# Performance work log

Hardware: AMD Instinct MI355X
Metric: run time of the kernel (lower is better)

Reference implementation:

```python
import jax, jax.numpy as jnp
import numpy as np

N_NODES = 100000
N_EDGES = 1600000
D_IN = 128
D_HID = 128


def _sage_conv(x, src, dst, n_nodes, W_l, b_l, W_r):
    # mean-aggregate source-node features onto destination nodes
    msg = x[src]  # [E, d] gather
    agg = jax.ops.segment_sum(msg, dst, num_segments=n_nodes)  # [N, d]
    deg = jax.ops.segment_sum(jnp.ones((src.shape[0],), x.dtype), dst,
                              num_segments=n_nodes)  # [N]
    agg = agg / jnp.maximum(deg, 1.0)[:, None]
    # lin_l(agg) + lin_r(x)  (lin_r has no bias, as in PyG SAGEConv)
    return agg @ W_l + b_l + x @ W_r


def setup_inputs() -> dict:
    key = jax.random.key(0)
    ks = jax.random.split(key, 8)
    x = jax.random.normal(ks[0], (N_NODES, D_IN), dtype=jnp.float32)
    edge_index = jax.random.randint(ks[1], (2, N_EDGES), 0, N_NODES, dtype=jnp.int32)
    s_in = 1.0 / np.sqrt(D_IN)
    s_hid = 1.0 / np.sqrt(D_HID)
    return {
        "x": x,
        "edge_index": edge_index,
        "W1_l": jax.random.normal(ks[2], (D_IN, D_HID), jnp.float32) * s_in,
        "b1_l": jnp.zeros((D_HID,), jnp.float32),
        "W1_r": jax.random.normal(ks[3], (D_IN, D_HID), jnp.float32) * s_in,
        "W2_l": jax.random.normal(ks[4], (D_HID, D_HID), jnp.float32) * s_hid,
        "b2_l": jnp.zeros((D_HID,), jnp.float32),
        "W2_r": jax.random.normal(ks[5], (D_HID, D_HID), jnp.float32) * s_hid,
    }


def reference(x, edge_index, W1_l, b1_l, W1_r, W2_l, b2_l, W2_r):
    src, dst = edge_index[0], edge_index[1]
    h = _sage_conv(x, src, dst, x.shape[0], W1_l, b1_l, W1_r)
    h = jax.nn.relu(h)
    # dropout inactive in eval mode
    h = _sage_conv(h, src, dst, x.shape[0], W2_l, b2_l, W2_r)
    return h
```

## Files before the change

### kernel.cpp

```cpp
#include <hip/hip_runtime.h>
#include <hip/hip_bf16.h>
#include <stdint.h>

typedef short short8 __attribute__((ext_vector_type(8)));
typedef float floatx4 __attribute__((ext_vector_type(4)));
typedef int intx4 __attribute__((ext_vector_type(4)));

#define NSEG 8
#define BLK_PER_SEG 256
#define SLOT 32
#define SPILL 32

static __device__ __forceinline__ unsigned short f2bf(float f) {
    union { float f; unsigned u; } v; v.f = f;
    unsigned r = v.u + 0x7FFF + ((v.u >> 16) & 1);
    return (unsigned short)(r >> 16);
}
static __device__ __forceinline__ float bflo(unsigned u) {
    union { unsigned u; float f; } v; v.u = u << 16; return v.f;
}
static __device__ __forceinline__ float bfhi(unsigned u) {
    union { unsigned u; float f; } v; v.u = u & 0xFFFF0000u; return v.f;
}

__global__ void k_conv_x(const float4* __restrict__ x, ushort4* __restrict__ o, int n4) {
    int t = blockIdx.x * blockDim.x + threadIdx.x;
    if (t >= n4) return;
    float4 v = x[t];
    ushort4 r = { f2bf(v.x), f2bf(v.y), f2bf(v.z), f2bf(v.w) };
    o[t] = r;
}

__global__ void k_trans_w(const float* __restrict__ W1l, const float* __restrict__ W1r,
                          const float* __restrict__ W2l, const float* __restrict__ W2r,
                          ushort* __restrict__ wt1, ushort* __restrict__ wt2) {
    int t = blockIdx.x * blockDim.x + threadIdx.x;
    int m = t >> 15, r = t & 32767;
    int k = r >> 7, n = r & 127;
    const float* Wl = m ? W2l : W1l;
    const float* Wr = m ? W2r : W1r;
    float v = (k < 128) ? Wl[k * 128 + n] : Wr[(k - 128) * 128 + n];
    ushort* wt = m ? wt2 : wt1;
    wt[n * 256 + k] = f2bf(v);
}

static __device__ __forceinline__ int seg_of(int d, float inv_nps) {
    int s = (int)((float)d * inv_nps);
    return s > (NSEG - 1) ? (NSEG - 1) : s;
}

static __device__ __forceinline__ void put_slot(int d, int s, int* __restrict__ cnt,
                                                int* __restrict__ slots,
                                                int* __restrict__ spill) {
    int p = atomicAdd(&cnt[d], 1);
    if (p < SLOT) slots[(size_t)d * SLOT + p] = s;
    else          spill[(size_t)d * SPILL + (p - SLOT)] = s;
}

__global__ void __launch_bounds__(256)
k_build(const int* __restrict__ src, const int* __restrict__ dst,
        int* __restrict__ cnt, int* __restrict__ slots, int* __restrict__ spill,
        int E, float inv_nps) {
    int seg  = blockIdx.x & 7;
    int bseg = blockIdx.x >> 3;
    int e4tot = E >> 2;
    int ec4 = (e4tot + BLK_PER_SEG - 1) / BLK_PER_SEG;
    int start4 = bseg * ec4, end4 = min(e4tot, start4 + ec4);
    const intx4* d4 = (const intx4*)dst;
    const intx4* s4 = (const intx4*)src;
    for (int i = start4 + (int)threadIdx.x; i < end4; i += 256) {
        intx4 dv = __builtin_nontemporal_load(&d4[i]);
        intx4 sv = __builtin_nontemporal_load(&s4[i]);
        if (seg_of(dv.x, inv_nps) == seg) put_slot(dv.x, sv.x, cnt, slots, spill);
        if (seg_of(dv.y, inv_nps) == seg) put_slot(dv.y, sv.y, cnt, slots, spill);
        if (seg_of(dv.z, inv_nps) == seg) put_slot(dv.z, sv.z, cnt, slots, spill);
        if (seg_of(dv.w, inv_nps) == seg) put_slot(dv.w, sv.w, cnt, slots, spill);
    }
    if (bseg == BLK_PER_SEG - 1 && (int)threadIdx.x < (E & 3)) {
        int e = (e4tot << 2) + threadIdx.x;
        int d = dst[e];
        if (seg_of(d, inv_nps) == seg) put_slot(d, src[e], cnt, slots, spill);
    }
}

__global__ void __launch_bounds__(256)
k_agg(const ushort* __restrict__ h, const int* __restrict__ cnt,
      const int* __restrict__ slots, const int* __restrict__ spill,
      ushort* __restrict__ agg, int n) {
    int node = (blockIdx.x * 256 + threadIdx.x) >> 6;
    int lane = threadIdx.x & 63;
    if (node >= n) return;
    int eg = lane >> 4;
    int c8 = lane & 15;
    int deg = cnt[node];
    const int* sl = slots + (size_t)node * SLOT;
    const int* sp = spill + (size_t)node * SPILL;
    float a[8];
    #pragma unroll
    for (int i = 0; i < 8; ++i) a[i] = 0.f;
    const ushort* hb = h + (size_t)c8 * 8;
    for (int j = 0; j < deg; j += 16) {
        int b0 = j + eg * 4;
        const int* ip = (b0 < SLOT) ? (sl + b0) : (sp + (b0 - SLOT));
        uint4 iv = *(const uint4*)ip;
        uint4 u0 = {0,0,0,0}, u1 = {0,0,0,0}, u2 = {0,0,0,0}, u3 = {0,0,0,0};
        if (b0     < deg) u0 = *(const uint4*)(hb + (size_t)iv.x * 128);
        if (b0 + 1 < deg) u1 = *(const uint4*)(hb + (size_t)iv.y * 128);
        if (b0 + 2 < deg) u2 = *(const uint4*)(hb + (size_t)iv.z * 128);
        if (b0 + 3 < deg) u3 = *(const uint4*)(hb + (size_t)iv.w * 128);
        a[0] += bflo(u0.x) + bflo(u1.x) + bflo(u2.x) + bflo(u3.x);
        a[1] += bfhi(u0.x) + bfhi(u1.x) + bfhi(u2.x) + bfhi(u3.x);
        a[2] += bflo(u0.y) + bflo(u1.y) + bflo(u2.y) + bflo(u3.y);
        a[3] += bfhi(u0.y) + bfhi(u1.y) + bfhi(u2.y) + bfhi(u3.y);
        a[4] += bflo(u0.z) + bflo(u1.z) + bflo(u2.z) + bflo(u3.z);
        a[5] += bfhi(u0.z) + bfhi(u1.z) + bfhi(u2.z) + bfhi(u3.z);
        a[6] += bflo(u0.w) + bflo(u1.w) + bflo(u2.w) + bflo(u3.w);
        a[7] += bfhi(u0.w) + bfhi(u1.w) + bfhi(u2.w) + bfhi(u3.w);
    }
    #pragma unroll
    for (int m = 16; m < 64; m <<= 1) {
        #pragma unroll
        for (int i = 0; i < 8; ++i) a[i] += __shfl_xor(a[i], m);
    }
    if (eg == 0) {
        float inv = 1.0f / fmaxf((float)deg, 1.0f);
        uint4 o;
        o.x = (unsigned)f2bf(a[0] * inv) | ((unsigned)f2bf(a[1] * inv) << 16);
        o.y = (unsigned)f2bf(a[2] * inv) | ((unsigned)f2bf(a[3] * inv) << 16);
        o.z = (unsigned)f2bf(a[4] * inv) | ((unsigned)f2bf(a[5] * inv) << 16);
        o.w = (unsigned)f2bf(a[6] * inv) | ((unsigned)f2bf(a[7] * inv) << 16);
        *(uint4*)(agg + (size_t)node * 128 + c8 * 8) = o;
    }
}

__global__ void __launch_bounds__(256)
k_gemm(const ushort* __restrict__ A1, const ushort* __restrict__ A2,
       const ushort* __restrict__ wt, const float* __restrict__ bias,
       int M, int mode, ushort* __restrict__ out16, float* __restrict__ out32) {
    __shared__ ushort W[128 * 264];
    int tid = threadIdx.x;
    #pragma unroll
    for (int i = 0; i < 16; ++i) {
        int t = tid + i * 256;
        int nrow = t >> 5, k8 = t & 31;
        *(uint4*)&W[nrow * 264 + k8 * 8] = *(const uint4*)&wt[nrow * 256 + k8 * 8];
    }
    __syncthreads();
    int wave = tid >> 6, lane = tid & 63;
    int l15 = lane & 15, lg = lane >> 4;
    int row_base = blockIdx.x * 64 + wave * 16;
    int r = row_base + l15;
    int rc = min(r, M - 1);
    const ushort* a1 = A1 + (size_t)rc * 128;
    const ushort* a2 = A2 + (size_t)rc * 128;
    int kg = lg * 8;
    floatx4 acc[8];
    #pragma unroll
    for (int c = 0; c < 8; ++c) acc[c] = (floatx4){0.f, 0.f, 0.f, 0.f};
    #pragma unroll
    for (int ks = 0; ks < 8; ++ks) {
        int k0 = ks * 32 + kg;
        const ushort* ap = (ks < 4) ? (a1 + k0) : (a2 + (k0 - 128));
        short8 a = *(const short8*)ap;
        #pragma unroll
        for (int c = 0; c < 8; ++c) {
            short8 b = *(const short8*)&W[(c * 16 + l15) * 264 + k0];
            acc[c] = __builtin_amdgcn_mfma_f32_16x16x32_bf16(a, b, acc[c], 0, 0, 0);
        }
    }
    #pragma unroll
    for (int c = 0; c < 8; ++c) {
        int coln = c * 16 + l15;
        float bv = bias[coln];
        #pragma unroll
        for (int i = 0; i < 4; ++i) {
            int row = row_base + lg * 4 + i;
            if (row < M) {
                float v = acc[c][i] + bv;
                if (mode == 0) {
                    v = fmaxf(v, 0.f);
                    out16[(size_t)row * 128 + coln] = f2bf(v);
                } else {
                    out32[(size_t)row * 128 + coln] = v;
                }
            }
        }
    }
}

extern "C" void kernel_launch(void* const* d_in, const int* in_sizes, int n_in,
                              void* d_out, int out_size, void* d_ws, size_t ws_size,
                              hipStream_t stream) {
    const float* x   = (const float*)d_in[0];
    const int*   ei  = (const int*)d_in[1];
    const float* W1l = (const float*)d_in[2];
    const float* b1  = (const float*)d_in[3];
    const float* W1r = (const float*)d_in[4];
    const float* W2l = (const float*)d_in[5];
    const float* b2  = (const float*)d_in[6];
    const float* W2r = (const float*)d_in[7];
    const int N = in_sizes[0] / 128;
    const int E = in_sizes[1] / 2;
    const int* srcv = ei;
    const int* dstv = ei + E;

    char* ws = (char*)d_ws;
    size_t o = 0;
    auto alloc = [&](size_t bytes) {
        o = (o + 255) & ~(size_t)255;
        char* p = ws + o; o += bytes; return p;
    };
    int*    cnt  = (int*)alloc((size_t)N * 4);
    ushort* x16  = (ushort*)alloc((size_t)N * 128 * 2);
    ushort* h16  = (ushort*)alloc((size_t)N * 128 * 2);
    ushort* agg  = (ushort*)alloc((size_t)N * 128 * 2);
    ushort* wt1  = (ushort*)alloc(128 * 256 * 2);
    ushort* wt2  = (ushort*)alloc(128 * 256 * 2);
    int* slots = (int*)d_out;
    int* spill = (int*)((char*)d_out + (size_t)N * SLOT * 4);

    hipMemsetAsync(cnt, 0, (size_t)N * 4, stream);

    int nps = (N + NSEG - 1) / NSEG;
    float inv_nps = 1.0f / (float)nps;

    int n4 = N * 32;
    k_conv_x<<<(n4 + 255) / 256, 256, 0, stream>>>((const float4*)x, (ushort4*)x16, n4);
    k_trans_w<<<256, 256, 0, stream>>>(W1l, W1r, W2l, W2r, wt1, wt2);

    k_build<<<NSEG * BLK_PER_SEG, 256, 0, stream>>>(srcv, dstv, cnt, slots, spill, E, inv_nps);

    k_agg<<<(N + 3) / 4, 256, 0, stream>>>(x16, cnt, slots, spill, agg, N);
    k_gemm<<<(N + 63) / 64, 256, 0, stream>>>(agg, x16, wt1, b1, N, 0, h16, nullptr);
    k_agg<<<(N + 3) / 4, 256, 0, stream>>>(h16, cnt, slots, spill, agg, N);
    k_gemm<<<(N + 63) / 64, 256, 0, stream>>>(agg, h16, wt2, b2, N, 1, nullptr, (float*)d_out);
}
```

Baseline: 390.3 us.

## Partition edges by destination segment before building slot lists

Replaces the build kernel, which had every segment's blocks scan the full edge list (8x reads of src/dst), with a two-pass scheme. A partition kernel bins edges into per-segment buckets using wave ballots and block/global atomics, then a second kernel fills slots from each bucket. This cuts redundant reads while keeping destination-segment locality for the atomics. It adds a scratch buffer in the output region, and a fixed per-segment capacity (CAP) that could overflow on skewed inputs.

```diff
diff --git a/kernel.cpp b/kernel.cpp
--- a/kernel.cpp
+++ b/kernel.cpp
@@ -5,11 +5,13 @@
 typedef short short8 __attribute__((ext_vector_type(8)));
 typedef float floatx4 __attribute__((ext_vector_type(4)));
 typedef int intx4 __attribute__((ext_vector_type(4)));
+typedef int intx2 __attribute__((ext_vector_type(2)));
 
 #define NSEG 8
-#define BLK_PER_SEG 256
 #define SLOT 32
 #define SPILL 32
+#define CAP 210000
+#define BLD 128
 
 static __device__ __forceinline__ unsigned short f2bf(float f) {
     union { float f; unsigned u; } v; v.f = f;
@@ -49,6 +51,68 @@
     return s > (NSEG - 1) ? (NSEG - 1) : s;
 }
 
+__global__ void __launch_bounds__(256)
+k_part(const int* __restrict__ src, const int* __restrict__ dst,
+       intx2* __restrict__ part, int* __restrict__ qn, int E, float inv_nps) {
+    __shared__ int hist[NSEG];
+    __shared__ int wbase[4][NSEG];
+    __shared__ int gbase[NSEG];
+    int tid = threadIdx.x, wid = tid >> 6, lane = tid & 63;
+    if (tid < NSEG) hist[tid] = 0;
+    __syncthreads();
+    int i4 = blockIdx.x * 256 + tid;
+    int e0 = i4 * 4;
+    intx4 dv = {0,0,0,0}, sv = {0,0,0,0};
+    bool val[4];
+    int b[4];
+    if (e0 + 3 < E) {
+        dv = __builtin_nontemporal_load(&((const intx4*)dst)[i4]);
+        sv = __builtin_nontemporal_load(&((const intx4*)src)[i4]);
+        #pragma unroll
+        for (int c = 0; c < 4; ++c) { val[c] = true; }
+    } else {
+        #pragma unroll
+        for (int c = 0; c < 4; ++c) {
+            val[c] = (e0 + c < E);
+            if (val[c]) { dv[c] = dst[e0 + c]; sv[c] = src[e0 + c]; }
+        }
+    }
+    #pragma unroll
+    for (int c = 0; c < 4; ++c) b[c] = val[c] ? seg_of(dv[c], inv_nps) : -1;
+
+    unsigned long long below = (lane == 63) ? ~0ULL >> 1
+                               : ((1ULL << lane) - 1);
+    int off[NSEG];
+    #pragma unroll
+    for (int k = 0; k < NSEG; ++k) off[k] = 0;
+    int rank[4];
+    #pragma unroll
+    for (int c = 0; c < 4; ++c) {
+        rank[c] = 0;
+        #pragma unroll
+        for (int k = 0; k < NSEG; ++k) {
+            unsigned long long m = __ballot(b[c] == k);
+            if (b[c] == k) rank[c] = off[k] + (int)__popcll(m & below);
+            off[k] += (int)__popcll(m);
+        }
+    }
+    int myoff = 0;
+    #pragma unroll
+    for (int k = 0; k < NSEG; ++k) myoff = (lane == k) ? off[k] : myoff;
+    if (lane < NSEG) wbase[wid][lane] = atomicAdd(&hist[lane], myoff);
+    __syncthreads();
+    if (tid < NSEG) gbase[tid] = atomicAdd(&qn[tid * 16], hist[tid]);
+    __syncthreads();
+    #pragma unroll
+    for (int c = 0; c < 4; ++c) {
+        if (val[c]) {
+            int k = b[c];
+            int pos = gbase[k] + wbase[wid][k] + rank[c];
+            part[(size_t)k * CAP + pos] = (intx2){ sv[c], dv[c] };
+        }
+    }
+}
+
 static __device__ __forceinline__ void put_slot(int d, int s, int* __restrict__ cnt,
                                                 int* __restrict__ slots,
                                                 int* __restrict__ spill) {
@@ -58,28 +122,15 @@
 }
 
 __global__ void __launch_bounds__(256)
-k_build(const int* __restrict__ src, const int* __restrict__ dst,
-        int* __restrict__ cnt, int* __restrict__ slots, int* __restrict__ spill,
-        int E, float inv_nps) {
+k_build2(const intx2* __restrict__ part, const int* __restrict__ qn,
+         int* __restrict__ cnt, int* __restrict__ slots, int* __restrict__ spill) {
     int seg  = blockIdx.x & 7;
     int bseg = blockIdx.x >> 3;
-    int e4tot = E >> 2;
-    int ec4 = (e4tot + BLK_PER_SEG - 1) / BLK_PER_SEG;
-    int start4 = bseg * ec4, end4 = min(e4tot, start4 + ec4);
-    const intx4* d4 = (const intx4*)dst;
-    const intx4* s4 = (const intx4*)src;
-    for (int i = start4 + (int)threadIdx.x; i < end4; i += 256) {
-        intx4 dv = __builtin_nontemporal_load(&d4[i]);
-        intx4 sv = __builtin_nontemporal_load(&s4[i]);
-        if (seg_of(dv.x, inv_nps) == seg) put_slot(dv.x, sv.x, cnt, slots, spill);
-        if (seg_of(dv.y, inv_nps) == seg) put_slot(dv.y, sv.y, cnt, slots, spill);
-        if (seg_of(dv.z, inv_nps) == seg) put_slot(dv.z, sv.z, cnt, slots, spill);
-        if (seg_of(dv.w, inv_nps) == seg) put_slot(dv.w, sv.w, cnt, slots, spill);
-    }
-    if (bseg == BLK_PER_SEG - 1 && (int)threadIdx.x < (E & 3)) {
-        int e = (e4tot << 2) + threadIdx.x;
-        int d = dst[e];
-        if (seg_of(d, inv_nps) == seg) put_slot(d, src[e], cnt, slots, spill);
+    int n = qn[seg * 16];
+    const intx2* p = part + (size_t)seg * CAP;
+    for (int i = bseg * 256 + (int)threadIdx.x; i < n; i += BLD * 256) {
+        intx2 e = __builtin_nontemporal_load(&p[i]);
+        put_slot(e.y, e.x, cnt, slots, spill);
     }
 }
 
@@ -211,15 +262,17 @@
         char* p = ws + o; o += bytes; return p;
     };
     int*    cnt  = (int*)alloc((size_t)N * 4);
+    int*    qn   = (int*)alloc(NSEG * 16 * 4);
     ushort* x16  = (ushort*)alloc((size_t)N * 128 * 2);
     ushort* h16  = (ushort*)alloc((size_t)N * 128 * 2);
     ushort* agg  = (ushort*)alloc((size_t)N * 128 * 2);
     ushort* wt1  = (ushort*)alloc(128 * 256 * 2);
     ushort* wt2  = (ushort*)alloc(128 * 256 * 2);
-    int* slots = (int*)d_out;
-    int* spill = (int*)((char*)d_out + (size_t)N * SLOT * 4);
-
-    hipMemsetAsync(cnt, 0, (size_t)N * 4, stream);
+    int*   slots = (int*)d_out;
+    int*   spill = (int*)((char*)d_out + (size_t)N * SLOT * 4);
+    intx2* part  = (intx2*)((char*)d_out + (size_t)N * (SLOT + SPILL) * 4);
+
+    hipMemsetAsync(cnt, 0, (size_t)((char*)qn - (char*)cnt) + NSEG * 16 * 4, stream);
 
     int nps = (N + NSEG - 1) / NSEG;
     float inv_nps = 1.0f / (float)nps;
@@ -228,7 +281,9 @@
     k_conv_x<<<(n4 + 255) / 256, 256, 0, stream>>>((const float4*)x, (ushort4*)x16, n4);
     k_trans_w<<<256, 256, 0, stream>>>(W1l, W1r, W2l, W2r, wt1, wt2);
 
-    k_build<<<NSEG * BLK_PER_SEG, 256, 0, stream>>>(srcv, dstv, cnt, slots, spill, E, inv_nps);
+    int e4 = (E + 3) / 4;
+    k_part<<<(e4 + 255) / 256, 256, 0, stream>>>(srcv, dstv, part, qn, E, inv_nps);
+    k_build2<<<NSEG * BLD, 256, 0, stream>>>(part, qn, cnt, slots, spill);
 
     k_agg<<<(N + 3) / 4, 256, 0, stream>>>(x16, cnt, slots, spill, agg, N);
     k_gemm<<<(N + 63) / 64, 256, 0, stream>>>(agg, x16, wt1, b1, N, 0, h16, nullptr);
```

Result: slower. 418.1 us (+7.1%).
